# Performance work log

Measured on AMD Instinct MI355X. Metric: run time of the kernel, lower is better.

## Reference

```python
import jax, jax.numpy as jnp
import numpy as np

B, H, W = 64, 480, 640
N_GROUPS, SAMPLE_PER_IMG = 100000, 3
NYU_FOCAL_AT_640 = 518.857


def setup_inputs() -> dict:
    key = jax.random.key(0)
    k1, k2, k3 = jax.random.split(key, 3)
    pred = jax.random.uniform(k1, (B, 1, H, W), dtype=jnp.float32, minval=0.05, maxval=1.0)
    gt = jax.random.uniform(k2, (B, 1, H, W), dtype=jnp.float32, minval=0.05, maxval=1.0)
    idx = jax.random.randint(k3, (B, N_GROUPS * SAMPLE_PER_IMG), 0, H * W, dtype=jnp.int32)
    return {"pred": pred, "gt": gt, "idx": idx}


def _unit_normals(points):
    # points: [B, G, 3(sample), 3(xyz)]
    a = points[:, :, 1] - points[:, :, 0]
    b = points[:, :, 2] - points[:, :, 0]
    n = jnp.cross(a, b)
    return n / (jnp.linalg.norm(n, axis=-1, keepdims=True) + 1e-8)


def reference(pred, gt, idx):
    Bb, _, Hh, Ww = pred.shape
    focal = NYU_FOCAL_AT_640 * (Ww / 640.0)
    cx, cy = Ww / 2.0, Hh / 2.0

    ys = (idx // Ww).astype(pred.dtype)          # [B, G*3]
    xs = (idx % Ww).astype(pred.dtype)
    X = (xs - cx) / focal
    Y = (ys - cy) / focal

    zp = jnp.take_along_axis(pred.reshape(Bb, -1), idx, axis=1)  # [B, G*3]
    zg = jnp.take_along_axis(gt.reshape(Bb, -1), idx, axis=1)

    pp = jnp.stack([X * zp, Y * zp, zp], axis=-1).reshape(Bb, N_GROUPS, SAMPLE_PER_IMG, 3)
    gg = jnp.stack([X * zg, Y * zg, zg], axis=-1).reshape(Bb, N_GROUPS, SAMPLE_PER_IMG, 3)

    np_ = _unit_normals(pp)  # [B, G, 3]
    ng_ = _unit_normals(gg)
    cos = jnp.clip(jnp.sum(np_ * ng_, axis=-1), -1.0, 1.0)  # [B, G]
    per_img = jnp.mean(1.0 - cos, axis=-1)                   # [B]
    return jnp.mean(per_img)
```

## Files before the change

kernel.cpp:

```cpp
#include <hip/hip_runtime.h>

#define BB   64
#define HH   480
#define WW   640
#define NG   100000
#define SPI  3
#define IMG  (HH * WW)
#define TPB  256
#define GPT  2
#define PPI  (NG / GPT)
#define BPI  ((PPI + TPB - 1) / TPB)
#define NXCD 8
#define IPX  (BB / NXCD)
#define JPX  (BPI * IPX)
#define GRID (JPX * NXCD)
#define FTPB 1024

__global__ __launch_bounds__(TPB) void vnl_main(
    const float* __restrict__ pred,
    const float* __restrict__ gt,
    const int*   __restrict__ idx,
    float*       __restrict__ partials)
{
    const int f    = blockIdx.x;
    const int xcd  = f & (NXCD - 1);
    const int j    = f >> 3;
    const int img  = xcd * IPX + j / BPI;
    const int chnk = j % BPI;
    const int q    = chnk * TPB + threadIdx.x;

    const float inv_f = 1.0f / 518.857f;
    const float cxc = 320.0f, cyc = 240.0f;

    float local = 0.0f;

    if (q < PPI) {
        const long long* ib =
            (const long long*)(idx + (size_t)img * (NG * SPI) + q * 6);
        long long w0 = __builtin_nontemporal_load(ib + 0);
        long long w1 = __builtin_nontemporal_load(ib + 1);
        long long w2 = __builtin_nontemporal_load(ib + 2);
        int ids[6] = {(int)(w0), (int)(w0 >> 32),
                      (int)(w1), (int)(w1 >> 32),
                      (int)(w2), (int)(w2 >> 32)};

        const float* pb = pred + (size_t)img * IMG;
        const float* gb = gt   + (size_t)img * IMG;

        float zp[6], zg[6];
        #pragma unroll
        for (int s = 0; s < 6; ++s) zp[s] = pb[ids[s]];
        #pragma unroll
        for (int s = 0; s < 6; ++s) zg[s] = gb[ids[s]];

        #pragma unroll
        for (int g = 0; g < GPT; ++g) {
            float X[3], Y[3];
            #pragma unroll
            for (int s = 0; s < 3; ++s) {
                int id = ids[g * 3 + s];
                int y  = id / WW;
                int x  = id - y * WW;
                X[s] = ((float)x - cxc) * inv_f;
                Y[s] = ((float)y - cyc) * inv_f;
            }
            const float* P = zp + g * 3;
            const float* G = zg + g * 3;

            float ax = X[1] * P[1] - X[0] * P[0], ay = Y[1] * P[1] - Y[0] * P[0], az = P[1] - P[0];
            float bx = X[2] * P[2] - X[0] * P[0], by = Y[2] * P[2] - Y[0] * P[0], bz = P[2] - P[0];
            float n1x = ay * bz - az * by;
            float n1y = az * bx - ax * bz;
            float n1z = ax * by - ay * bx;

            ax = X[1] * G[1] - X[0] * G[0]; ay = Y[1] * G[1] - Y[0] * G[0]; az = G[1] - G[0];
            bx = X[2] * G[2] - X[0] * G[0]; by = Y[2] * G[2] - Y[0] * G[0]; bz = G[2] - G[0];
            float n2x = ay * bz - az * by;
            float n2y = az * bx - ax * bz;
            float n2z = ax * by - ay * bx;

            float i1n = 1.0f / (sqrtf(n1x * n1x + n1y * n1y + n1z * n1z) + 1e-8f);
            float i2n = 1.0f / (sqrtf(n2x * n2x + n2y * n2y + n2z * n2z) + 1e-8f);
            float cosv = (n1x * n2x + n1y * n2y + n1z * n2z) * (i1n * i2n);
            cosv = fminf(1.0f, fmaxf(-1.0f, cosv));
            local += 1.0f - cosv;
        }
    }

    #pragma unroll
    for (int off = 32; off > 0; off >>= 1)
        local += __shfl_down(local, off, 64);

    __shared__ float wsum[TPB / 64];
    const int lane = threadIdx.x & 63;
    const int wid  = threadIdx.x >> 6;
    if (lane == 0) wsum[wid] = local;
    __syncthreads();

    if (threadIdx.x == 0)
        partials[f] = wsum[0] + wsum[1] + wsum[2] + wsum[3];
}

__global__ __launch_bounds__(FTPB) void vnl_final(
    const float* __restrict__ partials,
    float*       __restrict__ out)
{
    float s = 0.0f;
    for (int i = threadIdx.x; i < GRID; i += FTPB)
        s += partials[i];

    #pragma unroll
    for (int off = 32; off > 0; off >>= 1)
        s += __shfl_down(s, off, 64);

    __shared__ float wsum[FTPB / 64];
    const int lane = threadIdx.x & 63;
    const int wid  = threadIdx.x >> 6;
    if (lane == 0) wsum[wid] = s;
    __syncthreads();

    if (threadIdx.x == 0) {
        float t = 0.0f;
        #pragma unroll
        for (int w = 0; w < FTPB / 64; ++w) t += wsum[w];
        out[0] = t * (1.0f / ((float)BB * (float)NG));
    }
}

extern "C" void kernel_launch(void* const* d_in, const int* in_sizes, int n_in,
                              void* d_out, int out_size, void* d_ws, size_t ws_size,
                              hipStream_t stream)
{
    const float* pred = (const float*)d_in[0];
    const float* gt   = (const float*)d_in[1];
    const int*   idx  = (const int*)d_in[2];
    float* out      = (float*)d_out;
    float* partials = (float*)d_ws;

    vnl_main<<<dim3(GRID), TPB, 0, stream>>>(pred, gt, idx, partials);
    vnl_final<<<1, FTPB, 0, stream>>>(partials, out);
}
```

Before: 355.2 us.

## Interleave pred and gt into a paired buffer before gathering

Adds a pre-pass kernel that interleaves pred and gt into one float2 array in workspace. The main kernel then fetches each sampled pixel's predicted and ground-truth depth with a single 8-byte gather instead of two separate random loads. The goal is to halve the number of scattered memory transactions. In exchange, every call pays a full streaming read and write of both images (roughly 300MB of traffic). The path is only taken when the workspace is large enough; otherwise the original kernel runs.

```diff
diff --git a/kernel.cpp b/kernel.cpp
--- a/kernel.cpp
+++ b/kernel.cpp
@@ -15,6 +15,117 @@
 #define JPX  (BPI * IPX)
 #define GRID (JPX * NXCD)
 #define FTPB 1024
+#define ITPB 256
+#define IGRD 4096
+
+__device__ __forceinline__ float group_loss(
+    const float X[3], const float Y[3], const float P[3], const float G[3])
+{
+    float ax = X[1] * P[1] - X[0] * P[0], ay = Y[1] * P[1] - Y[0] * P[0], az = P[1] - P[0];
+    float bx = X[2] * P[2] - X[0] * P[0], by = Y[2] * P[2] - Y[0] * P[0], bz = P[2] - P[0];
+    float n1x = ay * bz - az * by;
+    float n1y = az * bx - ax * bz;
+    float n1z = ax * by - ay * bx;
+
+    ax = X[1] * G[1] - X[0] * G[0]; ay = Y[1] * G[1] - Y[0] * G[0]; az = G[1] - G[0];
+    bx = X[2] * G[2] - X[0] * G[0]; by = Y[2] * G[2] - Y[0] * G[0]; bz = G[2] - G[0];
+    float n2x = ay * bz - az * by;
+    float n2y = az * bx - ax * bz;
+    float n2z = ax * by - ay * bx;
+
+    float i1n = 1.0f / (sqrtf(n1x * n1x + n1y * n1y + n1z * n1z) + 1e-8f);
+    float i2n = 1.0f / (sqrtf(n2x * n2x + n2y * n2y + n2z * n2z) + 1e-8f);
+    float cosv = (n1x * n2x + n1y * n2y + n1z * n2z) * (i1n * i2n);
+    cosv = fminf(1.0f, fmaxf(-1.0f, cosv));
+    return 1.0f - cosv;
+}
+
+__device__ __forceinline__ void block_reduce_store(
+    float local, float* __restrict__ partials, int f)
+{
+    #pragma unroll
+    for (int off = 32; off > 0; off >>= 1)
+        local += __shfl_down(local, off, 64);
+
+    __shared__ float wsum[TPB / 64];
+    const int lane = threadIdx.x & 63;
+    const int wid  = threadIdx.x >> 6;
+    if (lane == 0) wsum[wid] = local;
+    __syncthreads();
+
+    if (threadIdx.x == 0)
+        partials[f] = wsum[0] + wsum[1] + wsum[2] + wsum[3];
+}
+
+__global__ __launch_bounds__(ITPB) void vnl_interleave(
+    const float4* __restrict__ pred,
+    const float4* __restrict__ gt,
+    float4*       __restrict__ pg)
+{
+    const size_t total = (size_t)BB * IMG / 4;
+    for (size_t u = (size_t)blockIdx.x * ITPB + threadIdx.x; u < total;
+         u += (size_t)gridDim.x * ITPB) {
+        float4 p = pred[u];
+        float4 g = gt[u];
+        float4 lo = make_float4(p.x, g.x, p.y, g.y);
+        float4 hi = make_float4(p.z, g.z, p.w, g.w);
+        pg[u * 2]     = lo;
+        pg[u * 2 + 1] = hi;
+    }
+}
+
+__global__ __launch_bounds__(TPB) void vnl_main_pg(
+    const float2* __restrict__ pg,
+    const int*    __restrict__ idx,
+    float*        __restrict__ partials)
+{
+    const int f    = blockIdx.x;
+    const int xcd  = f & (NXCD - 1);
+    const int j    = f >> 3;
+    const int img  = xcd * IPX + j / BPI;
+    const int chnk = j % BPI;
+    const int q    = chnk * TPB + threadIdx.x;
+
+    const float inv_f = 1.0f / 518.857f;
+    const float cxc = 320.0f, cyc = 240.0f;
+
+    float local = 0.0f;
+
+    if (q < PPI) {
+        const long long* ib =
+            (const long long*)(idx + (size_t)img * (NG * SPI) + q * 6);
+        long long w0 = __builtin_nontemporal_load(ib + 0);
+        long long w1 = __builtin_nontemporal_load(ib + 1);
+        long long w2 = __builtin_nontemporal_load(ib + 2);
+        int ids[6] = {(int)(w0), (int)(w0 >> 32),
+                      (int)(w1), (int)(w1 >> 32),
+                      (int)(w2), (int)(w2 >> 32)};
+
+        const float2* pgb = pg + (size_t)img * IMG;
+
+        float2 v[6];
+        #pragma unroll
+        for (int s = 0; s < 6; ++s) v[s] = pgb[ids[s]];
+
+        #pragma unroll
+        for (int g = 0; g < GPT; ++g) {
+            float X[3], Y[3], P[3], G[3];
+            #pragma unroll
+            for (int s = 0; s < 3; ++s) {
+                int id = ids[g * 3 + s];
+                int y  = id / WW;
+                int x  = id - y * WW;
+                X[s] = ((float)x - cxc) * inv_f;
+                Y[s] = ((float)y - cyc) * inv_f;
+                P[s] = v[g * 3 + s].x;
+                G[s] = v[g * 3 + s].y;
+            }
+            local += group_loss(X, Y, P, G);
+        }
+    }
+
+    block_reduce_store(local, partials, f);
+}
 
 __global__ __launch_bounds__(TPB) void vnl_main(
     const float* __restrict__ pred,
@@ -64,41 +175,11 @@
                 X[s] = ((float)x - cxc) * inv_f;
                 Y[s] = ((float)y - cyc) * inv_f;
             }
-            const float* P = zp + g * 3;
-            const float* G = zg + g * 3;
-
-            float ax = X[1] * P[1] - X[0] * P[0], ay = Y[1] * P[1] - Y[0] * P[0], az = P[1] - P[0];
-            float bx = X[2] * P[2] - X[0] * P[0], by = Y[2] * P[2] - Y[0] * P[0], bz = P[2] - P[0];
-            float n1x = ay * bz - az * by;
-            float n1y = az * bx - ax * bz;
-            float n1z = ax * by - ay * bx;
-
-            ax = X[1] * G[1] - X[0] * G[0]; ay = Y[1] * G[1] - Y[0] * G[0]; az = G[1] - G[0];
-            bx = X[2] * G[2] - X[0] * G[0]; by = Y[2] * G[2] - Y[0] * G[0]; bz = G[2] - G[0];
-            float n2x = ay * bz - az * by;
-            float n2y = az * bx - ax * bz;
-            float n2z = ax * by - ay * bx;
-
-            float i1n = 1.0f / (sqrtf(n1x * n1x + n1y * n1y + n1z * n1z) + 1e-8f);
-            float i2n = 1.0f / (sqrtf(n2x * n2x + n2y * n2y + n2z * n2z) + 1e-8f);
-            float cosv = (n1x * n2x + n1y * n2y + n1z * n2z) * (i1n * i2n);
-            cosv = fminf(1.0f, fmaxf(-1.0f, cosv));
-            local += 1.0f - cosv;
+            local += group_loss(X, Y, zp + g * 3, zg + g * 3);
         }
     }
 
-    #pragma unroll
-    for (int off = 32; off > 0; off >>= 1)
-        local += __shfl_down(local, off, 64);
-
-    __shared__ float wsum[TPB / 64];
-    const int lane = threadIdx.x & 63;
-    const int wid  = threadIdx.x >> 6;
-    if (lane == 0) wsum[wid] = local;
-    __syncthreads();
-
-    if (threadIdx.x == 0)
-        partials[f] = wsum[0] + wsum[1] + wsum[2] + wsum[3];
+    block_reduce_store(local, partials, f);
 }
 
 __global__ __launch_bounds__(FTPB) void vnl_final(
@@ -134,9 +215,21 @@
     const float* pred = (const float*)d_in[0];
     const float* gt   = (const float*)d_in[1];
     const int*   idx  = (const int*)d_in[2];
-    float* out      = (float*)d_out;
-    float* partials = (float*)d_ws;
-
-    vnl_main<<<dim3(GRID), TPB, 0, stream>>>(pred, gt, idx, partials);
-    vnl_final<<<1, FTPB, 0, stream>>>(partials, out);
-}
+    float* out = (float*)d_out;
+
+    const size_t pg_elems = (size_t)BB * IMG * 2;
+    const size_t need = pg_elems * sizeof(float) + GRID * sizeof(float);
+
+    if (ws_size >= need) {
+        float* pg       = (float*)d_ws;
+        float* partials = pg + pg_elems;
+        vnl_interleave<<<IGRD, ITPB, 0, stream>>>(
+            (const float4*)pred, (const float4*)gt, (float4*)pg);
+        vnl_main_pg<<<GRID, TPB, 0, stream>>>((const float2*)pg, idx, partials);
+        vnl_final<<<1, FTPB, 0, stream>>>(partials, out);
+    } else {
+        float* partials = (float*)d_ws;
+        vnl_main<<<GRID, TPB, 0, stream>>>(pred, gt, idx, partials);
+        vnl_final<<<1, FTPB, 0, stream>>>(partials, out);
+    }
+}
```

Result: faster. 344.1 us (-3.1%).
